# Performance work log

Hardware: AMD Instinct MI355X
Metric: run time of the kernel (lower is better)

Reference implementation:

```python
import jax, jax.numpy as jnp
import numpy as np

G_GRAPHS = 10000
K = 17  # keypoints per graph
# COCO-17 skeleton bones
SKEL = np.array([(15,13),(13,11),(16,14),(14,12),(11,12),(5,11),(6,12),(5,6),(5,7),
                 (6,8),(7,9),(8,10),(1,2),(0,1),(0,2),(1,3),(2,4),(3,5),(4,6)], dtype=np.int64)
DIMS = [2, 64, 64, 64, 128, 128, 128, 256, 256, 256]
BN_EPS = 1e-5


def setup_inputs() -> dict:
    key = jax.random.key(0)
    ks = jax.random.split(key, 16)
    N = G_GRAPHS * K
    # per-graph skeleton edges (bidirectional), offset per graph
    e = np.concatenate([SKEL, SKEL[:, ::-1]], axis=0)            # [38,2]
    off = np.arange(G_GRAPHS, dtype=np.int64)[:, None, None] * K
    edges = (e[None, :, :] + off).reshape(-1, 2)                 # [G*38, 2]
    inp = {
        'x': jax.random.normal(ks[0], (N, 2), jnp.float32),
        'att': jax.random.uniform(ks[1], (N, 1), jnp.float32),
        'edge_index': jnp.asarray(edges.T),                      # [2, E] int64->int32 ok
    }
    for i in range(9):
        kw = jax.random.fold_in(ks[2], i)
        scale = 1.0 / np.sqrt(DIMS[i])
        inp[f'W{i+1}'] = (jax.random.normal(kw, (DIMS[i], DIMS[i+1]), jnp.float32) * scale)
        inp[f'b{i+1}'] = jnp.zeros((DIMS[i+1],), jnp.float32)
    inp['fcW'] = jax.random.normal(ks[3], (6, 256, 256), jnp.float32) * (1.0 / 16.0)  # [scale,out,in]
    inp['fcB'] = jnp.zeros((6, 256), jnp.float32)
    inp['bn_gamma'] = jnp.ones((6, 256), jnp.float32)
    inp['bn_beta'] = jnp.zeros((6, 256), jnp.float32)
    inp['bn_rm'] = jnp.zeros((6, 256), jnp.float32)
    inp['bn_rv'] = jnpp if False else jnp.ones((6, 256), jnp.float32)
    return inp


def _forward(x, att, edge_index, Ws, bs, fcW, fcB, bn_gamma, bn_beta, bn_rm, bn_rv):
    N = x.shape[0]
    ar = jnp.arange(N, dtype=edge_index.dtype)
    src = jnp.concatenate([edge_index[0], ar])   # add self-loops (PyG GCNConv default)
    dst = jnp.concatenate([edge_index[1], ar])
    deg = jax.ops.segment_sum(jnp.ones_like(dst, dtype=jnp.float32), dst, num_segments=N)
    dinv = 1.0 / jnp.sqrt(deg)                   # deg >= 1 due to self-loops
    norm = (dinv[src] * dinv[dst])[:, None]      # [E+N, 1]

    h = x
    for W, b in zip(Ws, bs):
        msg = (h @ W)[src] * norm                # gather-linear-scale
        agg = jax.ops.segment_sum(msg, dst, num_segments=N)
        h = jnp.maximum((agg + b) * att, 0.0)    # AttGCNConv * att, then ReLU

    # JRPP pooling: [B, 17, 256] -> [B, 6, 256]
    xg = h.reshape(-1, K, h.shape[-1])
    g1 = xg.mean(axis=1, keepdims=True)
    g2 = jnp.concatenate([xg[:, :11].mean(1, keepdims=True),
                          xg[:, 11:].mean(1, keepdims=True)], axis=1)
    head = xg[:, jnp.array([0, 1, 2, 3, 4])].mean(1, keepdims=True)
    larl = xg[:, jnp.array([5, 7, 9, 12, 14, 16])].mean(1, keepdims=True)
    rall = xg[:, jnp.array([6, 8, 10, 11, 13, 15])].mean(1, keepdims=True)
    pooled = jnp.concatenate([g1, g2, head, larl, rall], axis=1)  # [B, 6, 256]

    # per-scale Linear (torch weight layout [out,in]) + eval-mode BatchNorm1d
    ft = jnp.einsum('bsi,soi->bso', pooled, fcW) + fcB
    fi = (ft - bn_rm) * (bn_gamma / jnp.sqrt(bn_rv + BN_EPS)) + bn_beta
    out = fi.reshape(fi.shape[0], -1)            # [B, 1536]
    # F.normalize(p=2, dim=1)
    nrm = jnp.maximum(jnp.linalg.norm(out, axis=1, keepdims=True), 1e-12)
    return out / nrm


def reference(x, att, edge_index, W1, b1, W2, b2, W3, b3, W4, b4, W5, b5, W6, b6,
              W7, b7, W8, b8, W9, b9, fcW, fcB, bn_gamma, bn_beta, bn_rm, bn_rv):
    Ws = [W1, W2, W3, W4, W5, W6, W7, W8, W9]
    bs = [b1, b2, b3, b4, b5, b6, b7, b8, b9]
    return _forward(x, att, edge_index, Ws, bs, fcW, fcB, bn_gamma, bn_beta, bn_rm, bn_rv)
```

## Files before the change

### kernel.cpp

```cpp
#include <hip/hip_runtime.h>
#include <math.h>


typedef _Float16 f16;
typedef _Float16 v2h __attribute__((ext_vector_type(2)));
typedef _Float16 v4h __attribute__((ext_vector_type(4)));
typedef _Float16 v8h __attribute__((ext_vector_type(8)));
typedef float    v4f __attribute__((ext_vector_type(4)));

namespace {

constexpr int BA[19] = {15,13,16,14,11, 5, 6, 5, 5, 6, 7, 8, 1, 0, 0, 1, 2, 3, 4};
constexpr int BB[19] = {13,11,14,12,12,11,12, 6, 7, 8, 9,10, 2, 1, 2, 3, 4, 5, 6};
constexpr float DINV[17] = {
  0.57735026919f, 0.5f, 0.5f, 0.57735026919f, 0.57735026919f,
  0.44721359550f, 0.44721359550f, 0.57735026919f, 0.57735026919f,
  0.70710678119f, 0.70710678119f, 0.5f, 0.5f,
  0.57735026919f, 0.57735026919f, 0.70710678119f, 0.70710678119f};

__device__ __forceinline__ int hswz(int row, int k){
  return row*256 + (k & ~63) + (((((k>>3)&7) ^ (row&7)))<<3) + (k&7);
}
__device__ __forceinline__ int zswz(int c, int r){
  return c*64 + (r ^ ((c&7)<<3));
}

__device__ __forceinline__ void ldh2(const f16* p, float* d){
  const v2h v = *(const v2h*)p; d[0]=v[0]; d[1]=v[1];
}

__device__ __forceinline__ v4h pk4(float a, float b, float c, float d){
  v4h o; o[0]=(f16)a; o[1]=(f16)b; o[2]=(f16)c; o[3]=(f16)d;
  return o;
}

template<int KP, int DOUT>
__device__ __forceinline__ void layer_phase(f16* __restrict__ H, f16* ztw,
    const f16* __restrict__ wp, const float* __restrict__ bias,
    const float (&av3)[3], const v8h (&Bfrag)[3][2],
    int w, int m, int q)
{
  constexpr int NKS = KP/32;
  constexpr int NTW = DOUT/64;
  constexpr int CT_PER = (NTW>=2)?2:1;
  constexpr int NPASS = NTW/CT_PER;

  v4f acc[3][NTW];
  #pragma unroll
  for (int a=0;a<3;++a)
    #pragma unroll
    for (int b=0;b<NTW;++b) acc[a][b] = v4f{0.f,0.f,0.f,0.f};

  #pragma unroll
  for (int ks=0; ks<NKS; ++ks){
    v8h af[3];
    #pragma unroll
    for (int mt=0;mt<3;++mt)
      af[mt] = *(const v8h*)(H + hswz(mt*16+m, ks*32 + q*8));
    #pragma unroll
    for (int nt=0;nt<NTW;++nt){
      const v8h bf = *(const v8h*)(wp + ((((w*NTW+nt)*NKS + ks)*64 + q*16 + m)<<3));
      #pragma unroll
      for (int mt=0;mt<3;++mt)
        acc[mt][nt] = __builtin_amdgcn_mfma_f32_16x16x32_f16(af[mt], bf, acc[mt][nt], 0,0,0);
    }
  }

  __syncthreads();

  #pragma unroll
  for (int p=0;p<NPASS;++p){
    #pragma unroll
    for (int nt2=0;nt2<CT_PER;++nt2){
      #pragma unroll
      for (int mt=0;mt<3;++mt){
        const v4f a4 = acc[mt][p*CT_PER+nt2];
        *(v4h*)(ztw + zswz(nt2*16+m, mt*16+q*4)) = pk4(a4[0],a4[1],a4[2],a4[3]);
      }
    }
    #pragma unroll
    for (int ct2=0;ct2<CT_PER;++ct2){
      const v8h za0 = *(const v8h*)(ztw + zswz(ct2*16+m, q*8));
      const v8h za1 = *(const v8h*)(ztw + zswz(ct2*16+m, 32 + q*8));
      v4f a2[3];
      #pragma unroll
      for (int mt=0;mt<3;++mt) a2[mt] = v4f{0.f,0.f,0.f,0.f};
      #pragma unroll
      for (int mt=0;mt<3;++mt)
        a2[mt] = __builtin_amdgcn_mfma_f32_16x16x32_f16(za0, Bfrag[mt][0], a2[mt], 0,0,0);
      #pragma unroll
      for (int mt=0;mt<3;++mt)
        a2[mt] = __builtin_amdgcn_mfma_f32_16x16x32_f16(za1, Bfrag[mt][1], a2[mt], 0,0,0);
      const int cb = w*(DOUT/4) + (p*CT_PER+ct2)*16 + q*4;
      const v4f b4 = *(const v4f*)(bias + cb);
      #pragma unroll
      for (int mt=0;mt<3;++mt){
        float f0 = fmaxf((a2[mt][0] + b4[0])*av3[mt], 0.f);
        float f1 = fmaxf((a2[mt][1] + b4[1])*av3[mt], 0.f);
        float f2 = fmaxf((a2[mt][2] + b4[2])*av3[mt], 0.f);
        float f3 = fmaxf((a2[mt][3] + b4[3])*av3[mt], 0.f);
        *(v4h*)(H + hswz(mt*16+m, cb)) = pk4(f0,f1,f2,f3);
      }
    }
  }
}

}

__global__ void prep_kernel(
    const float* __restrict__ W1, const float* __restrict__ W2,
    const float* __restrict__ W3, const float* __restrict__ W4,
    const float* __restrict__ W5, const float* __restrict__ W6,
    const float* __restrict__ W7, const float* __restrict__ W8,
    const float* __restrict__ W9,
    const float* __restrict__ B1, const float* __restrict__ B2,
    const float* __restrict__ B3, const float* __restrict__ B4,
    const float* __restrict__ B5, const float* __restrict__ B6,
    const float* __restrict__ B7, const float* __restrict__ B8,
    const float* __restrict__ B9,
    const float* __restrict__ fcW, const float* __restrict__ bng,
    const float* __restrict__ bnb, const float* __restrict__ bnrm,
    const float* __restrict__ bnrv, const float* __restrict__ att,
    f16* __restrict__ wt, f16* __restrict__ Ath, f16* __restrict__ fcWh,
    float* __restrict__ bnsc, float* __restrict__ bnsh,
    float* __restrict__ bcat, float* __restrict__ attp, int G)
{
  const int idx = blockIdx.x*blockDim.x + threadIdx.x;
  const int stride = gridDim.x*blockDim.x;
  const float* Ws[9] = {W1,W2,W3,W4,W5,W6,W7,W8,W9};
  const float* Bs[9] = {B1,B2,B3,B4,B5,B6,B7,B8,B9};
  const int DINs[9]  = {2,64,64,64,128,128,128,256,256};
  const int DOUTs[9] = {64,64,64,128,128,128,256,256,256};
  const int KPs[9]   = {32,64,64,64,128,128,128,256,256};
  const int OFFs[9]  = {0,2048,6144,10240,18432,34816,51200,83968,149504};
  const int BOFFs[9] = {0,64,128,192,320,448,576,832,1088};
  for (int l=0;l<9;++l){
    const float* W = Ws[l];
    const int DIN=DINs[l], DOUT=DOUTs[l], KP=KPs[l], NKS=KP>>5;
    f16* dst = wt + OFFs[l];
    const int n = DOUT*KP;
    for (int i=idx;i<n;i+=stride){
      const int jj = i&7, mm = (i>>3)&15, qq = (i>>7)&3, r2 = i>>9;
      const int ks = r2 & (NKS-1), ct = r2 / NKS;
      const int k = ks*32 + qq*8 + jj, c = ct*16 + mm;
      dst[i] = (k<DIN) ? (f16)W[k*DOUT + c] : (f16)0.f;
    }
    for (int i=idx;i<DOUT;i+=stride) bcat[BOFFs[l]+i] = Bs[l][i];
  }
  for (int i=idx;i<48*64;i+=stride){
    const int r = i>>6, j = i&63;
    float v = 0.f;
    if (j < 48 && ((r<24) == (j<24))){
      const int a = (r<24)? r : r-24;
      const int b = (j<24)? j : j-24;
      if (a<17 && b<17){
        bool adj = (a==b);
        #pragma unroll
        for (int e=0;e<19;++e)
          adj = adj || (BA[e]==a && BB[e]==b) || (BA[e]==b && BB[e]==a);
        if (adj) v = DINV[a]*DINV[b];
      }
    }
    Ath[i] = (f16)v;
  }
  for (int i=idx;i<6*256*256;i+=stride) fcWh[i] = (f16)fcW[i];
  for (int i=idx;i<1536;i+=stride){
    const float sc = bng[i] * rsqrtf(bnrv[i] + 1e-5f);
    bnsc[i] = sc; bnsh[i] = bnb[i] - bnrm[i]*sc;
  }
  const int G2 = (G+1)&~1;
  for (int i=idx;i<G2*24;i+=stride){
    const int g = i/24, j = i - g*24;
    attp[i] = (j<17 && g<G) ? att[(size_t)g*17 + j] : 0.f;
  }
}

__global__ __launch_bounds__(256, 3)
void gcn_kernel(const float* __restrict__ x, const f16* __restrict__ wt,
                const f16* __restrict__ Ath, const float* __restrict__ attp,
                const float* __restrict__ bcat,
                f16* __restrict__ pooled, int G)
{
  __shared__ __align__(16) f16 Hb[48*256];
  __shared__ __align__(16) f16 Zt[4*2048];
  const int t = threadIdx.x, w = t>>6, lane = t&63;
  const int m = lane&15, q = lane>>4;
  const int g0 = blockIdx.x*2;
  f16* ztw = Zt + w*2048;

  v8h Bfrag[3][2];
  #pragma unroll
  for (int mt=0;mt<3;++mt)
    #pragma unroll
    for (int ks2=0;ks2<2;++ks2)
      Bfrag[mt][ks2] = *(const v8h*)(Ath + (mt*16+m)*64 + ks2*32 + q*8);
  float av3[3];
  #pragma unroll
  for (int mt=0;mt<3;++mt) av3[mt] = attp[g0*24 + mt*16 + m];

  {
    const v8h z8 = {0,0,0,0,0,0,0,0};
    #pragma unroll
    for (int i=0;i<4;++i) *(v8h*)(Zt + t*32 + i*8) = z8;
    const int g = t>>7, kk = t&127;
    if (kk < 32){
      #pragma unroll
      for (int i=0;i<17;++i){
        float v = 0.f;
        if (kk < 2 && g0+g < G) v = x[(size_t)(g0+g)*34 + i*2 + kk];
        Hb[hswz(g*24+i, kk)] = (f16)v;
      }
      #pragma unroll
      for (int j=17;j<24;++j) Hb[hswz(g*24+j, kk)] = (f16)0.f;
    }
  }
  __syncthreads();

  layer_phase< 32, 64>(Hb, ztw, wt+0,      bcat+0,    av3, Bfrag, w, m, q); __syncthreads();
  layer_phase< 64, 64>(Hb, ztw, wt+2048,   bcat+64,   av3, Bfrag, w, m, q); __syncthreads();
  layer_phase< 64, 64>(Hb, ztw, wt+6144,   bcat+128,  av3, Bfrag, w, m, q); __syncthreads();
  layer_phase< 64,128>(Hb, ztw, wt+10240,  bcat+192,  av3, Bfrag, w, m, q); __syncthreads();
  layer_phase<128,128>(Hb, ztw, wt+18432,  bcat+320,  av3, Bfrag, w, m, q); __syncthreads();
  layer_phase<128,128>(Hb, ztw, wt+34816,  bcat+448,  av3, Bfrag, w, m, q); __syncthreads();
  layer_phase<128,256>(Hb, ztw, wt+51200,  bcat+576,  av3, Bfrag, w, m, q); __syncthreads();
  layer_phase<256,256>(Hb, ztw, wt+83968,  bcat+832,  av3, Bfrag, w, m, q); __syncthreads();
  layer_phase<256,256>(Hb, ztw, wt+149504, bcat+1088, av3, Bfrag, w, m, q); __syncthreads();

  const int g = t>>7, tt = t&127, k0 = tt*2, gg = g0 + g;
  if (gg < G){
    float sA[2]={0,0}, sB[2]={0,0}, sH[2]={0,0}, sL[2]={0,0}, sR[2]={0,0};
    #pragma unroll
    for (int i=0;i<17;++i){
      float hi[2];
      ldh2(&Hb[hswz(g*24+i, k0)], hi);
      #pragma unroll
      for (int v=0;v<2;++v){
        if (i<11) sA[v]+=hi[v]; else sB[v]+=hi[v];
        if (i<5)  sH[v]+=hi[v];
        if (i==5||i==7||i==9||i==12||i==14||i==16)  sL[v]+=hi[v];
        if (i==6||i==8||i==10||i==11||i==13||i==15) sR[v]+=hi[v];
      }
    }
    f16* op = pooled + (size_t)gg*1536 + k0;
    v2h o;
    #pragma unroll
    for (int v=0;v<2;++v) o[v]=(f16)((sA[v]+sB[v])*(1.0f/17.0f)); *(v2h*)(op+0*256)=o;
    #pragma unroll
    for (int v=0;v<2;++v) o[v]=(f16)(sA[v]*(1.0f/11.0f));         *(v2h*)(op+1*256)=o;
    #pragma unroll
    for (int v=0;v<2;++v) o[v]=(f16)(sB[v]*(1.0f/6.0f));          *(v2h*)(op+2*256)=o;
    #pragma unroll
    for (int v=0;v<2;++v) o[v]=(f16)(sH[v]*(1.0f/5.0f));          *(v2h*)(op+3*256)=o;
    #pragma unroll
    for (int v=0;v<2;++v) o[v]=(f16)(sL[v]*(1.0f/6.0f));          *(v2h*)(op+4*256)=o;
    #pragma unroll
    for (int v=0;v<2;++v) o[v]=(f16)(sR[v]*(1.0f/6.0f));          *(v2h*)(op+5*256)=o;
  }
}

__global__ __launch_bounds__(256, 2)
void head_kernel(const f16* __restrict__ pooled, const f16* __restrict__ fcWh,
                 const float* __restrict__ fcB, const float* __restrict__ bnsc,
                 const float* __restrict__ bnsh, float* __restrict__ out, int G)
{
  __shared__ __align__(16) f16 Ap[16*1536];
  __shared__ float red[64];
  __shared__ float invn[16];
  const int t = threadIdx.x, w = t>>6, lane = t&63;
  const int m = lane&15, q = lane>>4;
  const int g0 = blockIdx.x*16;
  const int cb = w*64;

  for (int id=t; id<16*192; id+=256){
    const int row = id/192, cc = id - row*192;
    v8h v = v8h{0,0,0,0,0,0,0,0};
    const int gg = g0 + row;
    if (gg < G) v = *(const v8h*)(pooled + (size_t)gg*1536 + cc*8);
    const int pc = (cc & ~7) | ((cc&7) ^ (row&7));
    *(v8h*)(Ap + row*1536 + pc*8) = v;
  }
  __syncthreads();

  v4f acc[6][4];
  #pragma unroll
  for (int s=0;s<6;++s)
    #pragma unroll
    for (int nt=0;nt<4;++nt) acc[s][nt] = v4f{0.f,0.f,0.f,0.f};

  #pragma unroll
  for (int s=0;s<6;++s){
    #pragma unroll
    for (int ks=0; ks<8; ++ks){
      const int c = s*32 + ks*4 + q;
      const v8h af = *(const v8h*)(Ap + m*1536 + ((c & ~7) | ((c&7) ^ (m&7)))*8);
      #pragma unroll
      for (int nt=0;nt<4;++nt){
        const v8h bf = *(const v8h*)(fcWh + (size_t)(s*256 + cb + nt*16 + m)*256 + ks*32 + q*8);
        acc[s][nt] = __builtin_amdgcn_mfma_f32_16x16x32_f16(af, bf, acc[s][nt], 0,0,0);
      }
    }
  }

  float ss[4] = {0.f,0.f,0.f,0.f};
  #pragma unroll
  for (int s=0;s<6;++s)
    #pragma unroll
    for (int nt=0;nt<4;++nt){
      const int idx = s*256 + cb + nt*16 + m;
      const float bc = fcB[idx], sc = bnsc[idx], sh = bnsh[idx];
      #pragma unroll
      for (int i=0;i<4;++i){
        const float f = (acc[s][nt][i] + bc)*sc + sh;
        acc[s][nt][i] = f;
        ss[i] += f*f;
      }
    }

  #pragma unroll
  for (int off=1; off<16; off<<=1)
    #pragma unroll
    for (int i=0;i<4;++i) ss[i] += __shfl_xor(ss[i], off, 64);
  if (m==0)
    #pragma unroll
    for (int i=0;i<4;++i) red[w*16 + q*4 + i] = ss[i];
  __syncthreads();
  if (t < 16){
    const float s4 = red[t] + red[16+t] + red[32+t] + red[48+t];
    invn[t] = 1.f / fmaxf(sqrtf(s4), 1e-12f);
  }
  __syncthreads();
  float iv[4];
  #pragma unroll
  for (int i=0;i<4;++i) iv[i] = invn[q*4+i];
  #pragma unroll
  for (int s=0;s<6;++s)
    #pragma unroll
    for (int nt=0;nt<4;++nt)
      #pragma unroll
      for (int i=0;i<4;++i){
        const int gg = g0 + q*4 + i;
        if (gg < G)
          out[(size_t)gg*1536 + s*256 + cb + nt*16 + m] = acc[s][nt][i]*iv[i];
      }
}

extern "C" void kernel_launch(void* const* d_in, const int* in_sizes, int n_in,
                              void* d_out, int out_size, void* d_ws, size_t ws_size,
                              hipStream_t stream) {
  (void)n_in; (void)out_size; (void)ws_size;
  const float* x   = (const float*)d_in[0];
  const float* att = (const float*)d_in[1];
  const float* W[9]; const float* B[9];
  for (int i=0;i<9;i++){ W[i]=(const float*)d_in[3+2*i]; B[i]=(const float*)d_in[4+2*i]; }
  const float* fcW  = (const float*)d_in[21];
  const float* fcB  = (const float*)d_in[22];
  const float* bn_g = (const float*)d_in[23];
  const float* bn_b = (const float*)d_in[24];
  const float* bn_rm= (const float*)d_in[25];
  const float* bn_rv= (const float*)d_in[26];
  float* out = (float*)d_out;

  const int G = in_sizes[1] / 17;
  const int G2 = (G+1)&~1;

  char* ws = (char*)d_ws;
  f16*   wt   = (f16*)(ws);
  f16*   fcWh = (f16*)(ws + 430080);
  float* bnsc = (float*)(ws + 1216512);
  float* bnsh = (float*)(ws + 1222656);
  float* bcat = (float*)(ws + 1228800);
  f16*   Ath  = (f16*)(ws + 1234176);
  float* attp = (float*)(ws + 1240320);
  size_t poolOff = (1240320 + (size_t)G2*96 + 255) & ~(size_t)255;
  f16* pooled = (f16*)(ws + poolOff);

  prep_kernel<<<256, 256, 0, stream>>>(
      W[0],W[1],W[2],W[3],W[4],W[5],W[6],W[7],W[8],
      B[0],B[1],B[2],B[3],B[4],B[5],B[6],B[7],B[8],
      fcW, bn_g, bn_b, bn_rm, bn_rv, att,
      wt, Ath, fcWh, bnsc, bnsh, bcat, attp, G);

  const int gb = (G + 1) / 2;
  gcn_kernel<<<gb, 256, 0, stream>>>(
      x, wt, Ath, attp, bcat, pooled, G);

  head_kernel<<<(G + 15)/16, 256, 0, stream>>>(
      pooled, fcWh, fcB, bnsc, bnsh, out, G);
}
```

Measured before the change: 387.6 us.

## Give each wavefront its own graph and drop block-wide barriers in GCN layers

Work in the GCN kernel moves from two graphs per block shared across four waves to one graph per wave (four per block). Each wave now holds its graph's 32-row activation tile in LDS and computes every output column itself, so all the __syncthreads between layers go away and the normalized adjacency shrinks to a 32x32 block. In exchange each wave streams the full weight matrix for each layer instead of a quarter of it, so per-graph weight traffic rises, and LDS per block grows, with the launch bound lowered from 3 to 2 blocks per CU.

```diff
diff --git a/kernel.cpp b/kernel.cpp
--- a/kernel.cpp
+++ b/kernel.cpp
@@ -22,11 +22,7 @@
   return row*256 + (k & ~63) + (((((k>>3)&7) ^ (row&7)))<<3) + (k&7);
 }
 __device__ __forceinline__ int zswz(int c, int r){
-  return c*64 + (r ^ ((c&7)<<3));
-}
-
-__device__ __forceinline__ void ldh2(const f16* p, float* d){
-  const v2h v = *(const v2h*)p; d[0]=v[0]; d[1]=v[1];
+  return c*32 + (r ^ ((c&3)<<3));
 }
 
 __device__ __forceinline__ v4h pk4(float a, float b, float c, float d){
@@ -35,72 +31,56 @@
 }
 
 template<int KP, int DOUT>
-__device__ __forceinline__ void layer_phase(f16* __restrict__ H, f16* ztw,
-    const f16* __restrict__ wp, const float* __restrict__ bias,
-    const float (&av3)[3], const v8h (&Bfrag)[3][2],
-    int w, int m, int q)
+__device__ __forceinline__ void layer_phase(f16* __restrict__ H,
+    f16* __restrict__ zt, const f16* __restrict__ wp,
+    const float* __restrict__ bias, const float (&av)[2],
+    const v8h (&Bfrag)[2], int m, int q)
 {
   constexpr int NKS = KP/32;
-  constexpr int NTW = DOUT/64;
-  constexpr int CT_PER = (NTW>=2)?2:1;
-  constexpr int NPASS = NTW/CT_PER;
-
-  v4f acc[3][NTW];
-  #pragma unroll
-  for (int a=0;a<3;++a)
+  constexpr int NTW = DOUT/16;
+
+  v4f acc[2][NTW];
+  #pragma unroll
+  for (int a=0;a<2;++a)
     #pragma unroll
     for (int b=0;b<NTW;++b) acc[a][b] = v4f{0.f,0.f,0.f,0.f};
 
   #pragma unroll
   for (int ks=0; ks<NKS; ++ks){
-    v8h af[3];
-    #pragma unroll
-    for (int mt=0;mt<3;++mt)
-      af[mt] = *(const v8h*)(H + hswz(mt*16+m, ks*32 + q*8));
-    #pragma unroll
-    for (int nt=0;nt<NTW;++nt){
-      const v8h bf = *(const v8h*)(wp + ((((w*NTW+nt)*NKS + ks)*64 + q*16 + m)<<3));
-      #pragma unroll
-      for (int mt=0;mt<3;++mt)
-        acc[mt][nt] = __builtin_amdgcn_mfma_f32_16x16x32_f16(af[mt], bf, acc[mt][nt], 0,0,0);
-    }
-  }
-
-  __syncthreads();
-
-  #pragma unroll
-  for (int p=0;p<NPASS;++p){
-    #pragma unroll
-    for (int nt2=0;nt2<CT_PER;++nt2){
-      #pragma unroll
-      for (int mt=0;mt<3;++mt){
-        const v4f a4 = acc[mt][p*CT_PER+nt2];
-        *(v4h*)(ztw + zswz(nt2*16+m, mt*16+q*4)) = pk4(a4[0],a4[1],a4[2],a4[3]);
-      }
-    }
-    #pragma unroll
-    for (int ct2=0;ct2<CT_PER;++ct2){
-      const v8h za0 = *(const v8h*)(ztw + zswz(ct2*16+m, q*8));
-      const v8h za1 = *(const v8h*)(ztw + zswz(ct2*16+m, 32 + q*8));
-      v4f a2[3];
-      #pragma unroll
-      for (int mt=0;mt<3;++mt) a2[mt] = v4f{0.f,0.f,0.f,0.f};
-      #pragma unroll
-      for (int mt=0;mt<3;++mt)
-        a2[mt] = __builtin_amdgcn_mfma_f32_16x16x32_f16(za0, Bfrag[mt][0], a2[mt], 0,0,0);
-      #pragma unroll
-      for (int mt=0;mt<3;++mt)
-        a2[mt] = __builtin_amdgcn_mfma_f32_16x16x32_f16(za1, Bfrag[mt][1], a2[mt], 0,0,0);
-      const int cb = w*(DOUT/4) + (p*CT_PER+ct2)*16 + q*4;
-      const v4f b4 = *(const v4f*)(bias + cb);
-      #pragma unroll
-      for (int mt=0;mt<3;++mt){
-        float f0 = fmaxf((a2[mt][0] + b4[0])*av3[mt], 0.f);
-        float f1 = fmaxf((a2[mt][1] + b4[1])*av3[mt], 0.f);
-        float f2 = fmaxf((a2[mt][2] + b4[2])*av3[mt], 0.f);
-        float f3 = fmaxf((a2[mt][3] + b4[3])*av3[mt], 0.f);
-        *(v4h*)(H + hswz(mt*16+m, cb)) = pk4(f0,f1,f2,f3);
-      }
+    const v8h af0 = *(const v8h*)(H + hswz(m,      ks*32 + q*8));
+    const v8h af1 = *(const v8h*)(H + hswz(16 + m, ks*32 + q*8));
+    #pragma unroll
+    for (int ct=0; ct<NTW; ++ct){
+      const v8h bf = *(const v8h*)(wp + ((ct*NKS + ks)*64 + q*16 + m)*8);
+      acc[0][ct] = __builtin_amdgcn_mfma_f32_16x16x32_f16(af0, bf, acc[0][ct], 0,0,0);
+      acc[1][ct] = __builtin_amdgcn_mfma_f32_16x16x32_f16(af1, bf, acc[1][ct], 0,0,0);
+    }
+  }
+
+  #pragma unroll
+  for (int ct=0; ct<NTW; ++ct){
+    f16* zs = zt + (ct&1)*512;
+    *(v4h*)(zs + zswz(m, q*4))      = pk4(acc[0][ct][0],acc[0][ct][1],acc[0][ct][2],acc[0][ct][3]);
+    *(v4h*)(zs + zswz(m, 16 + q*4)) = pk4(acc[1][ct][0],acc[1][ct][1],acc[1][ct][2],acc[1][ct][3]);
+    const v8h za = *(const v8h*)(zs + zswz(m, q*8));
+    const v4f z4 = v4f{0.f,0.f,0.f,0.f};
+    const v4f a20 = __builtin_amdgcn_mfma_f32_16x16x32_f16(za, Bfrag[0], z4, 0,0,0);
+    const v4f a21 = __builtin_amdgcn_mfma_f32_16x16x32_f16(za, Bfrag[1], z4, 0,0,0);
+    const int c0 = ct*16 + q*4;
+    const v4f b4 = *(const v4f*)(bias + c0);
+    {
+      const float f0 = fmaxf((a20[0]+b4[0])*av[0], 0.f);
+      const float f1 = fmaxf((a20[1]+b4[1])*av[0], 0.f);
+      const float f2 = fmaxf((a20[2]+b4[2])*av[0], 0.f);
+      const float f3 = fmaxf((a20[3]+b4[3])*av[0], 0.f);
+      *(v4h*)(H + hswz(m, c0)) = pk4(f0,f1,f2,f3);
+    }
+    {
+      const float f0 = fmaxf((a21[0]+b4[0])*av[1], 0.f);
+      const float f1 = fmaxf((a21[1]+b4[1])*av[1], 0.f);
+      const float f2 = fmaxf((a21[2]+b4[2])*av[1], 0.f);
+      const float f3 = fmaxf((a21[3]+b4[3])*av[1], 0.f);
+      *(v4h*)(H + hswz(16 + m, c0)) = pk4(f0,f1,f2,f3);
     }
   }
 }
@@ -121,7 +101,7 @@
     const float* __restrict__ fcW, const float* __restrict__ bng,
     const float* __restrict__ bnb, const float* __restrict__ bnrm,
     const float* __restrict__ bnrv, const float* __restrict__ att,
-    f16* __restrict__ wt, f16* __restrict__ Ath, f16* __restrict__ fcWh,
+    f16* __restrict__ wt, f16* __restrict__ At32, f16* __restrict__ fcWh,
     float* __restrict__ bnsc, float* __restrict__ bnsh,
     float* __restrict__ bcat, float* __restrict__ attp, int G)
 {
@@ -147,114 +127,97 @@
     }
     for (int i=idx;i<DOUT;i+=stride) bcat[BOFFs[l]+i] = Bs[l][i];
   }
-  for (int i=idx;i<48*64;i+=stride){
-    const int r = i>>6, j = i&63;
+  for (int i=idx;i<32*32;i+=stride){
+    const int r = i>>5, j = i&31;
     float v = 0.f;
-    if (j < 48 && ((r<24) == (j<24))){
-      const int a = (r<24)? r : r-24;
-      const int b = (j<24)? j : j-24;
-      if (a<17 && b<17){
-        bool adj = (a==b);
-        #pragma unroll
-        for (int e=0;e<19;++e)
-          adj = adj || (BA[e]==a && BB[e]==b) || (BA[e]==b && BB[e]==a);
-        if (adj) v = DINV[a]*DINV[b];
-      }
-    }
-    Ath[i] = (f16)v;
+    if (r<17 && j<17){
+      bool adj = (r==j);
+      #pragma unroll
+      for (int e=0;e<19;++e)
+        adj = adj || (BA[e]==r && BB[e]==j) || (BA[e]==j && BB[e]==r);
+      if (adj) v = DINV[r]*DINV[j];
+    }
+    At32[i] = (f16)v;
   }
   for (int i=idx;i<6*256*256;i+=stride) fcWh[i] = (f16)fcW[i];
   for (int i=idx;i<1536;i+=stride){
     const float sc = bng[i] * rsqrtf(bnrv[i] + 1e-5f);
     bnsc[i] = sc; bnsh[i] = bnb[i] - bnrm[i]*sc;
   }
-  const int G2 = (G+1)&~1;
-  for (int i=idx;i<G2*24;i+=stride){
-    const int g = i/24, j = i - g*24;
+  const int G4 = (G+3)&~3;
+  for (int i=idx;i<G4*32;i+=stride){
+    const int g = i>>5, j = i&31;
     attp[i] = (j<17 && g<G) ? att[(size_t)g*17 + j] : 0.f;
   }
 }
 
-__global__ __launch_bounds__(256, 3)
+__global__ __launch_bounds__(256, 2)
 void gcn_kernel(const float* __restrict__ x, const f16* __restrict__ wt,
-                const f16* __restrict__ Ath, const float* __restrict__ attp,
+                const f16* __restrict__ At32, const float* __restrict__ attp,
                 const float* __restrict__ bcat,
                 f16* __restrict__ pooled, int G)
 {
-  __shared__ __align__(16) f16 Hb[48*256];
-  __shared__ __align__(16) f16 Zt[4*2048];
+  __shared__ __align__(16) f16 Hb[4][32*256];
+  __shared__ __align__(16) f16 Zs[4][2*512];
   const int t = threadIdx.x, w = t>>6, lane = t&63;
   const int m = lane&15, q = lane>>4;
-  const int g0 = blockIdx.x*2;
-  f16* ztw = Zt + w*2048;
-
-  v8h Bfrag[3][2];
-  #pragma unroll
-  for (int mt=0;mt<3;++mt)
-    #pragma unroll
-    for (int ks2=0;ks2<2;++ks2)
-      Bfrag[mt][ks2] = *(const v8h*)(Ath + (mt*16+m)*64 + ks2*32 + q*8);
-  float av3[3];
-  #pragma unroll
-  for (int mt=0;mt<3;++mt) av3[mt] = attp[g0*24 + mt*16 + m];
+  const int gg = blockIdx.x*4 + w;
+  const bool live = (gg < G);
+  f16* H  = Hb[w];
+  f16* zt = Zs[w];
+
+  v8h Bfrag[2];
+  Bfrag[0] = *(const v8h*)(At32 + (m)*32      + q*8);
+  Bfrag[1] = *(const v8h*)(At32 + (16+m)*32   + q*8);
+  float av[2];
+  av[0] = live ? attp[(size_t)gg*32 + m]      : 0.f;
+  av[1] = live ? attp[(size_t)gg*32 + 16 + m] : 0.f;
 
   {
-    const v8h z8 = {0,0,0,0,0,0,0,0};
-    #pragma unroll
-    for (int i=0;i<4;++i) *(v8h*)(Zt + t*32 + i*8) = z8;
-    const int g = t>>7, kk = t&127;
-    if (kk < 32){
-      #pragma unroll
-      for (int i=0;i<17;++i){
-        float v = 0.f;
-        if (kk < 2 && g0+g < G) v = x[(size_t)(g0+g)*34 + i*2 + kk];
-        Hb[hswz(g*24+i, kk)] = (f16)v;
+    const int c = lane & 31, rh = (lane>>5)*16;
+    #pragma unroll
+    for (int r=0;r<16;++r){
+      const int rr = rh + r;
+      float v = 0.f;
+      if (live && c < 2 && rr < 17) v = x[(size_t)gg*34 + rr*2 + c];
+      H[hswz(rr, c)] = (f16)v;
+    }
+  }
+
+  layer_phase< 32, 64>(H, zt, wt+0,      bcat+0,    av, Bfrag, m, q);
+  layer_phase< 64, 64>(H, zt, wt+2048,   bcat+64,   av, Bfrag, m, q);
+  layer_phase< 64, 64>(H, zt, wt+6144,   bcat+128,  av, Bfrag, m, q);
+  layer_phase< 64,128>(H, zt, wt+10240,  bcat+192,  av, Bfrag, m, q);
+  layer_phase<128,128>(H, zt, wt+18432,  bcat+320,  av, Bfrag, m, q);
+  layer_phase<128,128>(H, zt, wt+34816,  bcat+448,  av, Bfrag, m, q);
+  layer_phase<128,256>(H, zt, wt+51200,  bcat+576,  av, Bfrag, m, q);
+  layer_phase<256,256>(H, zt, wt+83968,  bcat+832,  av, Bfrag, m, q);
+  layer_phase<256,256>(H, zt, wt+149504, bcat+1088, av, Bfrag, m, q);
+
+  if (live){
+    const int k0 = lane*4;
+    float sA[4]={0,0,0,0}, sB[4]={0,0,0,0}, sH[4]={0,0,0,0},
+          sL[4]={0,0,0,0}, sR[4]={0,0,0,0};
+    #pragma unroll
+    for (int i=0;i<17;++i){
+      const v4h h4 = *(const v4h*)(H + hswz(i, k0));
+      #pragma unroll
+      for (int v=0;v<4;++v){
+        const float hv = (float)h4[v];
+        if (i<11) sA[v]+=hv; else sB[v]+=hv;
+        if (i<5)  sH[v]+=hv;
+        if (i==5||i==7||i==9||i==12||i==14||i==16)  sL[v]+=hv;
+        if (i==6||i==8||i==10||i==11||i==13||i==15) sR[v]+=hv;
       }
-      #pragma unroll
-      for (int j=17;j<24;++j) Hb[hswz(g*24+j, kk)] = (f16)0.f;
-    }
-  }
-  __syncthreads();
-
-  layer_phase< 32, 64>(Hb, ztw, wt+0,      bcat+0,    av3, Bfrag, w, m, q); __syncthreads();
-  layer_phase< 64, 64>(Hb, ztw, wt+2048,   bcat+64,   av3, Bfrag, w, m, q); __syncthreads();
-  layer_phase< 64, 64>(Hb, ztw, wt+6144,   bcat+128,  av3, Bfrag, w, m, q); __syncthreads();
-  layer_phase< 64,128>(Hb, ztw, wt+10240,  bcat+192,  av3, Bfrag, w, m, q); __syncthreads();
-  layer_phase<128,128>(Hb, ztw, wt+18432,  bcat+320,  av3, Bfrag, w, m, q); __syncthreads();
-  layer_phase<128,128>(Hb, ztw, wt+34816,  bcat+448,  av3, Bfrag, w, m, q); __syncthreads();
-  layer_phase<128,256>(Hb, ztw, wt+51200,  bcat+576,  av3, Bfrag, w, m, q); __syncthreads();
-  layer_phase<256,256>(Hb, ztw, wt+83968,  bcat+832,  av3, Bfrag, w, m, q); __syncthreads();
-  layer_phase<256,256>(Hb, ztw, wt+149504, bcat+1088, av3, Bfrag, w, m, q); __syncthreads();
-
-  const int g = t>>7, tt = t&127, k0 = tt*2, gg = g0 + g;
-  if (gg < G){
-    float sA[2]={0,0}, sB[2]={0,0}, sH[2]={0,0}, sL[2]={0,0}, sR[2]={0,0};
-    #pragma unroll
-    for (int i=0;i<17;++i){
-      float hi[2];
-      ldh2(&Hb[hswz(g*24+i, k0)], hi);
-      #pragma unroll
-      for (int v=0;v<2;++v){
-        if (i<11) sA[v]+=hi[v]; else sB[v]+=hi[v];
-        if (i<5)  sH[v]+=hi[v];
-        if (i==5||i==7||i==9||i==12||i==14||i==16)  sL[v]+=hi[v];
-        if (i==6||i==8||i==10||i==11||i==13||i==15) sR[v]+=hi[v];
-      }
     }
     f16* op = pooled + (size_t)gg*1536 + k0;
-    v2h o;
-    #pragma unroll
-    for (int v=0;v<2;++v) o[v]=(f16)((sA[v]+sB[v])*(1.0f/17.0f)); *(v2h*)(op+0*256)=o;
-    #pragma unroll
-    for (int v=0;v<2;++v) o[v]=(f16)(sA[v]*(1.0f/11.0f));         *(v2h*)(op+1*256)=o;
-    #pragma unroll
-    for (int v=0;v<2;++v) o[v]=(f16)(sB[v]*(1.0f/6.0f));          *(v2h*)(op+2*256)=o;
-    #pragma unroll
-    for (int v=0;v<2;++v) o[v]=(f16)(sH[v]*(1.0f/5.0f));          *(v2h*)(op+3*256)=o;
-    #pragma unroll
-    for (int v=0;v<2;++v) o[v]=(f16)(sL[v]*(1.0f/6.0f));          *(v2h*)(op+4*256)=o;
-    #pragma unroll
-    for (int v=0;v<2;++v) o[v]=(f16)(sR[v]*(1.0f/6.0f));          *(v2h*)(op+5*256)=o;
+    *(v4h*)(op+0*256) = pk4((sA[0]+sB[0])*(1.f/17.f),(sA[1]+sB[1])*(1.f/17.f),
+                            (sA[2]+sB[2])*(1.f/17.f),(sA[3]+sB[3])*(1.f/17.f));
+    *(v4h*)(op+1*256) = pk4(sA[0]*(1.f/11.f),sA[1]*(1.f/11.f),sA[2]*(1.f/11.f),sA[3]*(1.f/11.f));
+    *(v4h*)(op+2*256) = pk4(sB[0]*(1.f/6.f), sB[1]*(1.f/6.f), sB[2]*(1.f/6.f), sB[3]*(1.f/6.f));
+    *(v4h*)(op+3*256) = pk4(sH[0]*(1.f/5.f), sH[1]*(1.f/5.f), sH[2]*(1.f/5.f), sH[3]*(1.f/5.f));
+    *(v4h*)(op+4*256) = pk4(sL[0]*(1.f/6.f), sL[1]*(1.f/6.f), sL[2]*(1.f/6.f), sL[3]*(1.f/6.f));
+    *(v4h*)(op+5*256) = pk4(sR[0]*(1.f/6.f), sR[1]*(1.f/6.f), sR[2]*(1.f/6.f), sR[3]*(1.f/6.f));
   }
 }
 
@@ -361,7 +324,7 @@
   float* out = (float*)d_out;
 
   const int G = in_sizes[1] / 17;
-  const int G2 = (G+1)&~1;
+  const int G4 = (G+3)&~3;
 
   char* ws = (char*)d_ws;
   f16*   wt   = (f16*)(ws);
@@ -369,20 +332,20 @@
   float* bnsc = (float*)(ws + 1216512);
   float* bnsh = (float*)(ws + 1222656);
   float* bcat = (float*)(ws + 1228800);
-  f16*   Ath  = (f16*)(ws + 1234176);
-  float* attp = (float*)(ws + 1240320);
-  size_t poolOff = (1240320 + (size_t)G2*96 + 255) & ~(size_t)255;
+  f16*   At32 = (f16*)(ws + 1234176);
+  float* attp = (float*)(ws + 1236224);
+  size_t poolOff = (1236224 + (size_t)G4*128 + 255) & ~(size_t)255;
   f16* pooled = (f16*)(ws + poolOff);
 
   prep_kernel<<<256, 256, 0, stream>>>(
       W[0],W[1],W[2],W[3],W[4],W[5],W[6],W[7],W[8],
       B[0],B[1],B[2],B[3],B[4],B[5],B[6],B[7],B[8],
       fcW, bn_g, bn_b, bn_rm, bn_rv, att,
-      wt, Ath, fcWh, bnsc, bnsh, bcat, attp, G);
-
-  const int gb = (G + 1) / 2;
+      wt, At32, fcWh, bnsc, bnsh, bcat, attp, G);
+
+  const int gb = (G + 3) / 4;
   gcn_kernel<<<gb, 256, 0, stream>>>(
-      x, wt, Ath, attp, bcat, pooled, G);
+      x, wt, At32, attp, bcat, pooled, G);
 
   head_kernel<<<(G + 15)/16, 256, 0, stream>>>(
       pooled, fcWh, fcB, bnsc, bnsh, out, G);
```

After: 595.0 us. +53.5%, slower.
